# Kernel optimization log

Hardware: AMD Instinct MI355X
Metric: run time of the kernel (lower is better)

## Reference

```python
import jax, jax.numpy as jnp
import numpy as np

B, K, HH, WW = 512, 256, 16, 16   # batch, channels (K//2 of init K=512), latent H, W
KH = 128                          # GRU hidden size
F = 16                            # future_window_lin


def gru_forward(seq, h0, W_ih, W_hh, b_ih, b_hh):
    # seq: (B,T,K) batch_first, h0: (B,KH). PyTorch GRU gate order: r, z, n.
    gx = jnp.einsum('btk,gk->btg', seq, W_ih) + b_ih  # (B,T,3*KH)

    def step(h, gx_t):
        gh = h @ W_hh.T + b_hh
        xr, xz, xn = jnp.split(gx_t, 3, axis=-1)
        hr, hz, hn = jnp.split(gh, 3, axis=-1)
        r = jax.nn.sigmoid(xr + hr)
        z = jax.nn.sigmoid(xz + hz)
        n = jnp.tanh(xn + r * hn)
        h_new = (1.0 - z) * n + z * h
        return h_new, h_new

    hT, outs = jax.lax.scan(step, h0, jnp.swapaxes(gx, 0, 1))  # outs: (T,B,KH)
    return jnp.swapaxes(outs, 0, 1), hT


def setup_inputs() -> dict:
    key = jax.random.key(0)
    ks = jax.random.split(key, 9)
    s = 0.05
    return {
        'z_q_x_st': jax.random.normal(ks[0], (B, K, HH, WW), jnp.float32),
        'z_e_x': jax.random.normal(ks[1], (B, K, HH, WW), jnp.float32),
        'z_q_x': jax.random.normal(ks[2], (B, K, HH, WW), jnp.float32),
        'hidden': jnp.zeros((1, B, KH), jnp.float32),
        'W_ih': jax.random.normal(ks[3], (3 * KH, K), jnp.float32) * s,
        'W_hh': jax.random.normal(ks[4], (3 * KH, KH), jnp.float32) * s,
        'b_ih': jnp.zeros((3 * KH,), jnp.float32),
        'b_hh': jnp.zeros((3 * KH,), jnp.float32),
        'Wk_w': jax.random.normal(ks[5], (F, K, KH), jnp.float32) * s,
        'Wk_b': jnp.zeros((F, K), jnp.float32),
        'p_sample': 100,
    }


def reference(z_q_x_st, z_e_x, z_q_x, hidden, W_ih, W_hh, b_ih, b_hh, Wk_w, Wk_b, p_sample):
    batch, k, h, w = z_e_x.shape
    f = Wk_w.shape[0]
    # (B,K,H,W) -> (B,H*W,K); row = idx//W, col = idx%W is just the row-major flat index
    z_flat = jnp.transpose(z_q_x_st, (0, 2, 3, 1)).reshape(batch, h * w, k)
    # encoded samples at flat positions p_sample+1 .. p_sample+F  -> (F,B,K)
    encoded = jnp.swapaxes(z_flat[:, p_sample + 1: p_sample + 1 + f, :], 0, 1)
    # GRU over the causal prefix; c_t = output at step p_sample (the last one)
    seq = z_flat[:, : p_sample + 1, :]
    out, _ = gru_forward(seq, hidden[0], W_ih, W_hh, b_ih, b_hh)
    c_t = out[:, -1, :]  # (B,KH)
    # per-step linear heads, batched: (F,B,K)
    pred = jnp.einsum('fkh,bh->fbk', Wk_w, c_t) + Wk_b[:, None, :]
    # totals[i] = encoded[i] @ pred[i].T  -> (F,B,B)
    totals = jnp.einsum('fbk,fck->fbc', encoded, pred)
    lsm = jax.nn.log_softmax(totals, axis=2)
    diag_sum = jnp.sum(jnp.diagonal(lsm, axis1=1, axis2=2))
    nce = -diag_sum / (batch * f)
    # 'correct' only reflects the last loop iteration in the torch code
    last = totals[-1]
    sm = jax.nn.softmax(last, axis=1)       # softmax over dim=1, then argmax over dim=0
    preds_idx = jnp.argmax(sm, axis=0)
    correct = jnp.sum(preds_idx == jnp.arange(batch))
    accuracy = correct.astype(jnp.float32) / batch
    return accuracy, nce, z_e_x, z_q_x
```

## Files before the change

kernel.cpp:

```cpp
#include <hip/hip_runtime.h>
#include <math.h>

#define NB_B   512
#define NK     256
#define NKH    128
#define NG3    384
#define NT     101
#define NF     16
#define NPASS  (512ull*256*256)

#define OFF_GX   0ull
#define N_GX     (512ull*101*384)
#define OFF_CT   (OFF_GX + N_GX)
#define OFF_ENC  (OFF_CT + 512ull*128)
#define OFF_PRED (OFF_ENC + 16ull*512*256)
#define OFF_TOT  (OFF_PRED + 16ull*512*256)
#define OFF_LSE  (OFF_TOT + 16ull*512*512)
#define OFF_DML  (OFF_LSE + 8192ull)
#define OFF_WT   (OFF_DML + 8192ull)
#define OFF_WKT  (OFF_WT + 384ull*256)
#define OFF_CNT  (OFF_WKT + 16ull*128*256)

__global__ __launch_bounds__(256) void k_transpose(
    const float* __restrict__ W_ih, const float* __restrict__ Wk_w,
    float* __restrict__ Wt, float* __restrict__ Wkt, int* __restrict__ cnt) {
  int idx = blockIdx.x * 256 + threadIdx.x;
  if (idx == 0) *cnt = 0;
  if (idx < 384 * 256) {
    int g = idx % 384, k = idx / 384;
    Wt[idx] = W_ih[g * 256 + k];
  }
  if (idx < 16 * 128 * 256) {
    int k = idx & 255, h = (idx >> 8) & 127, f = idx >> 15;
    Wkt[idx] = Wk_w[(f * 256 + k) * 128 + h];
  }
}

__global__ __launch_bounds__(768) void k_gx(
    const float* __restrict__ zq, const float* __restrict__ Wt,
    const float* __restrict__ b_ih, float* __restrict__ gx) {
  __shared__ float Xs[32][104];
  __shared__ float Ws[32 * 384];
  int b = blockIdx.x;
  int tid = threadIdx.x;
  int q = tid % 96;
  int tt = tid / 96;
  int g0 = q * 4;
  int t0 = tt * 13;
  int lane = tid & 63, wid = tid >> 6;
  float acc[4][13];
#pragma unroll
  for (int i = 0; i < 4; i++)
#pragma unroll
    for (int j = 0; j < 13; j++) acc[i][j] = 0.f;
  const float* zb = zq + (size_t)b * 65536;
  for (int kc = 0; kc < 8; kc++) {
    __syncthreads();
    for (int k = wid; k < 32; k += 12) {
      int kk = kc * 32 + k;
      Xs[k][lane] = zb[kk * 256 + lane];
      int t1 = 64 + lane;
      if (t1 < 104) Xs[k][t1] = (t1 < 101) ? zb[kk * 256 + t1] : 0.f;
    }
    {
      const float4* wsrc = (const float4*)(Wt + (size_t)kc * 32 * 384);
      float4* wdst = (float4*)Ws;
      for (int i = tid; i < 3072; i += 768) wdst[i] = wsrc[i];
    }
    __syncthreads();
    for (int k = 0; k < 32; k++) {
      float4 w = *(const float4*)&Ws[k * 384 + g0];
      const float* xr = &Xs[k][t0];
#pragma unroll
      for (int j = 0; j < 13; j++) {
        float x = xr[j];
        acc[0][j] += w.x * x;
        acc[1][j] += w.y * x;
        acc[2][j] += w.z * x;
        acc[3][j] += w.w * x;
      }
    }
  }
  float4 bias = *(const float4*)&b_ih[g0];
#pragma unroll
  for (int j = 0; j < 13; j++) {
    int t = t0 + j;
    if (t < 101) {
      float4 v = make_float4(acc[0][j] + bias.x, acc[1][j] + bias.y,
                             acc[2][j] + bias.z, acc[3][j] + bias.w);
      *(float4*)&gx[(size_t)t * (512 * 384) + b * 384 + g0] = v;
    }
  }
}

__global__ __launch_bounds__(768) void k_scan(
    const float* __restrict__ gx, const float* __restrict__ W_hh,
    const float* __restrict__ b_hh, const float* __restrict__ hidden,
    float* __restrict__ ct,
    const float* __restrict__ src0, const float* __restrict__ src1,
    float2* __restrict__ d0, float2* __restrict__ d1) {
  int tid = threadIdx.x;
  if (blockIdx.x >= 256) {
    const float2* S0 = (const float2*)src0;
    const float2* S1 = (const float2*)src1;
    const size_t half = NPASS / 4;
    const size_t stride = 256ull * 768;
    for (size_t i = (size_t)(blockIdx.x - 256) * 768 + tid; i < half; i += stride) {
      float2 a = S0[i];
      float2 b2 = S0[i + half];
      float2 c = S1[i];
      float2 d = S1[i + half];
      d0[i] = a;
      d0[i + half] = b2;
      d1[i] = c;
      d1[i + half] = d;
    }
    return;
  }
  __shared__ float hs[2][128];
  __shared__ float ghp[2][2][384];
  int b0 = blockIdx.x * 2;
  int g = tid % 384, kh = tid / 384;
  float4 w[16];
  const float4* wp = (const float4*)(W_hh + g * 128 + kh * 64);
#pragma unroll
  for (int i = 0; i < 16; i++) w[i] = wp[i];
  if (tid < 256) {
    int r = tid >> 7, k = tid & 127;
    hs[r][k] = hidden[(b0 + r) * 128 + k];
  }
  __syncthreads();
  for (int t = 0; t < 101; t++) {
    const float4* h0 = (const float4*)&hs[0][kh * 64];
    const float4* h1 = (const float4*)&hs[1][kh * 64];
    float a0 = 0.f, a1 = 0.f;
#pragma unroll
    for (int i = 0; i < 16; i++) {
      float4 wv = w[i], x0 = h0[i], x1 = h1[i];
      a0 += wv.x * x0.x + wv.y * x0.y + wv.z * x0.z + wv.w * x0.w;
      a1 += wv.x * x1.x + wv.y * x1.y + wv.z * x1.z + wv.w * x1.w;
    }
    ghp[0][kh][g] = a0;
    ghp[1][kh][g] = a1;
    __syncthreads();
    if (tid < 256) {
      int r = tid >> 7, k = tid & 127;
      const float* gxb = gx + (size_t)t * (512 * 384) + (b0 + r) * 384;
      float xr = gxb[k], xz = gxb[128 + k], xn = gxb[256 + k];
      float hr = ghp[r][0][k] + ghp[r][1][k] + b_hh[k];
      float hz = ghp[r][0][128 + k] + ghp[r][1][128 + k] + b_hh[128 + k];
      float hn = ghp[r][0][256 + k] + ghp[r][1][256 + k] + b_hh[256 + k];
      float rr = 1.f / (1.f + __expf(-(xr + hr)));
      float zz = 1.f / (1.f + __expf(-(xz + hz)));
      float nn = tanhf(xn + rr * hn);
      hs[r][k] = (1.f - zz) * nn + zz * hs[r][k];
    }
    __syncthreads();
  }
  if (tid < 256) {
    int r = tid >> 7, k = tid & 127;
    ct[(b0 + r) * 128 + k] = hs[r][k];
  }
}

__global__ __launch_bounds__(256) void k_enc(const float* __restrict__ zq,
                                             float* __restrict__ enc) {
  __shared__ float tile[256][17];
  int b = blockIdx.x, tid = threadIdx.x;
  const float* zb = zq + (size_t)b * 65536;
  for (int pass = 0; pass < 16; pass++) {
    int idx = pass * 256 + tid;
    int k = idx >> 4, f = idx & 15;
    tile[k][f] = zb[k * 256 + 101 + f];
  }
  __syncthreads();
  for (int f = 0; f < 16; f++)
    enc[(size_t)f * 131072 + b * 256 + tid] = tile[tid][f];
}

__global__ __launch_bounds__(256) void k_pred(
    const float* __restrict__ Wkt, const float* __restrict__ Wk_b,
    const float* __restrict__ ct, float* __restrict__ pred) {
  __shared__ float cts[32][128];
  int f = blockIdx.x, c0 = blockIdx.y * 32;
  int tid = threadIdx.x;
  for (int pass = 0; pass < 16; pass++) {
    int idx = pass * 256 + tid;
    int cc = idx >> 7, h = idx & 127;
    cts[cc][h] = ct[(c0 + cc) * 128 + h];
  }
  __syncthreads();
  float acc[32];
#pragma unroll
  for (int i = 0; i < 32; i++) acc[i] = 0.f;
  const float* wb = Wkt + (size_t)f * 32768 + tid;
  for (int h = 0; h < 128; h += 4) {
    float w0 = wb[(h + 0) * 256], w1 = wb[(h + 1) * 256];
    float w2 = wb[(h + 2) * 256], w3 = wb[(h + 3) * 256];
#pragma unroll
    for (int cc = 0; cc < 32; cc++) {
      float4 cv = *(const float4*)&cts[cc][h];
      acc[cc] += w0 * cv.x + w1 * cv.y + w2 * cv.z + w3 * cv.w;
    }
  }
  float bias = Wk_b[f * 256 + tid];
#pragma unroll
  for (int cc = 0; cc < 32; cc++)
    pred[((size_t)f * 512 + c0 + cc) * 256 + tid] = acc[cc] + bias;
}

__global__ __launch_bounds__(256) void k_totals(
    const float* __restrict__ enc, const float* __restrict__ pred,
    float* __restrict__ tot) {
  __shared__ float As[32][68];
  __shared__ float Bs[32][68];
  int f = blockIdx.z, b0 = blockIdx.y * 64, c0 = blockIdx.x * 64;
  int tid = threadIdx.x;
  int tx = tid & 15, ty = tid >> 4;
  float acc[4][4];
#pragma unroll
  for (int i = 0; i < 4; i++)
#pragma unroll
    for (int j = 0; j < 4; j++) acc[i][j] = 0.f;
  const float* Ab = enc + (size_t)f * 131072;
  const float* Bb = pred + (size_t)f * 131072;
  int lr = tid >> 3;
  int lc = (tid & 7) * 4;
  for (int kc = 0; kc < 8; kc++) {
    int k0 = kc * 32;
    __syncthreads();
    float4 av0 = *(const float4*)&Ab[(b0 + lr) * 256 + k0 + lc];
    float4 av1 = *(const float4*)&Ab[(b0 + 32 + lr) * 256 + k0 + lc];
    float4 bv0 = *(const float4*)&Bb[(c0 + lr) * 256 + k0 + lc];
    float4 bv1 = *(const float4*)&Bb[(c0 + 32 + lr) * 256 + k0 + lc];
    As[lc + 0][lr] = av0.x; As[lc + 1][lr] = av0.y;
    As[lc + 2][lr] = av0.z; As[lc + 3][lr] = av0.w;
    As[lc + 0][lr + 32] = av1.x; As[lc + 1][lr + 32] = av1.y;
    As[lc + 2][lr + 32] = av1.z; As[lc + 3][lr + 32] = av1.w;
    Bs[lc + 0][lr] = bv0.x; Bs[lc + 1][lr] = bv0.y;
    Bs[lc + 2][lr] = bv0.z; Bs[lc + 3][lr] = bv0.w;
    Bs[lc + 0][lr + 32] = bv1.x; Bs[lc + 1][lr + 32] = bv1.y;
    Bs[lc + 2][lr + 32] = bv1.z; Bs[lc + 3][lr + 32] = bv1.w;
    __syncthreads();
#pragma unroll
    for (int kk = 0; kk < 32; kk++) {
      float4 a = *(const float4*)&As[kk][ty * 4];
      float4 bq = *(const float4*)&Bs[kk][tx * 4];
      acc[0][0] += a.x * bq.x; acc[0][1] += a.x * bq.y;
      acc[0][2] += a.x * bq.z; acc[0][3] += a.x * bq.w;
      acc[1][0] += a.y * bq.x; acc[1][1] += a.y * bq.y;
      acc[1][2] += a.y * bq.z; acc[1][3] += a.y * bq.w;
      acc[2][0] += a.z * bq.x; acc[2][1] += a.z * bq.y;
      acc[2][2] += a.z * bq.z; acc[2][3] += a.z * bq.w;
      acc[3][0] += a.w * bq.x; acc[3][1] += a.w * bq.y;
      acc[3][2] += a.w * bq.z; acc[3][3] += a.w * bq.w;
    }
  }
#pragma unroll
  for (int i = 0; i < 4; i++) {
    float4 v = make_float4(acc[i][0], acc[i][1], acc[i][2], acc[i][3]);
    *(float4*)&tot[(size_t)f * 262144 + (b0 + ty * 4 + i) * 512 + c0 + tx * 4] = v;
  }
}

__global__ __launch_bounds__(64) void k_lse(const float* __restrict__ tot,
                                            float* __restrict__ lse,
                                            float* __restrict__ dml) {
  int row = blockIdx.x;
  int b = row & 511;
  int lane = threadIdx.x;
  const float* tr = tot + (size_t)row * 512;
  float v[8];
  float mx = -1e30f;
#pragma unroll
  for (int i = 0; i < 8; i++) { v[i] = tr[i * 64 + lane]; mx = fmaxf(mx, v[i]); }
#pragma unroll
  for (int s = 32; s > 0; s >>= 1) mx = fmaxf(mx, __shfl_xor(mx, s));
  float sum = 0.f;
#pragma unroll
  for (int i = 0; i < 8; i++) sum += __expf(v[i] - mx);
#pragma unroll
  for (int s = 32; s > 0; s >>= 1) sum += __shfl_xor(sum, s);
  if (lane == 0) {
    float l = __logf(sum) + mx;
    lse[row] = l;
    dml[row] = tr[b] - l;
  }
}

__global__ __launch_bounds__(64) void k_acc(const float* __restrict__ tot,
                                            const float* __restrict__ lse,
                                            int* __restrict__ cnt) {
  int c = blockIdx.x;
  int lane = threadIdx.x;
  const float* t15 = tot + (size_t)15 * 262144;
  const float* l15 = lse + 15 * 512;
  float best = -1e30f;
  int bi = 1 << 30;
  for (int b = lane; b < 512; b += 64) {
    float v = t15[(size_t)b * 512 + c] - l15[b];
    if (v > best) { best = v; bi = b; }
  }
  for (int s = 32; s > 0; s >>= 1) {
    float ov = __shfl_xor(best, s);
    int oi = __shfl_xor(bi, s);
    if (ov > best || (ov == best && oi < bi)) { best = ov; bi = oi; }
  }
  if (lane == 0 && bi == c) atomicAdd(cnt, 1);
}

__global__ __launch_bounds__(256) void k_fin(const float* __restrict__ dml,
                                             const int* __restrict__ cnt,
                                             float* __restrict__ out) {
  __shared__ float red[256];
  int tid = threadIdx.x;
  float s = 0.f;
  for (int i = tid; i < 8192; i += 256) s += dml[i];
  red[tid] = s;
  __syncthreads();
  for (int st = 128; st > 0; st >>= 1) {
    if (tid < st) red[tid] += red[tid + st];
    __syncthreads();
  }
  if (tid == 0) {
    out[1] = -red[0] / 8192.f;
    out[0] = (float)(*cnt) / 512.f;
  }
}

extern "C" void kernel_launch(void* const* d_in, const int* in_sizes, int n_in,
                              void* d_out, int out_size, void* d_ws, size_t ws_size,
                              hipStream_t stream) {
  const float* zq   = (const float*)d_in[0];
  const float* ze   = (const float*)d_in[1];
  const float* zqx  = (const float*)d_in[2];
  const float* hid  = (const float*)d_in[3];
  const float* W_ih = (const float*)d_in[4];
  const float* W_hh = (const float*)d_in[5];
  const float* b_ih = (const float*)d_in[6];
  const float* b_hh = (const float*)d_in[7];
  const float* Wk_w = (const float*)d_in[8];
  const float* Wk_b = (const float*)d_in[9];
  float* out = (float*)d_out;
  float* ws  = (float*)d_ws;

  k_transpose<<<2048, 256, 0, stream>>>(W_ih, Wk_w, ws + OFF_WT, ws + OFF_WKT,
                                        (int*)(ws + OFF_CNT));
  k_gx<<<512, 768, 0, stream>>>(zq, ws + OFF_WT, b_ih, ws + OFF_GX);
  k_scan<<<512, 768, 0, stream>>>(ws + OFF_GX, W_hh, b_hh, hid, ws + OFF_CT,
                                  ze, zqx,
                                  (float2*)(out + 2), (float2*)(out + 2 + NPASS));
  k_enc<<<512, 256, 0, stream>>>(zq, ws + OFF_ENC);
  k_pred<<<dim3(16, 16), 256, 0, stream>>>(ws + OFF_WKT, Wk_b, ws + OFF_CT, ws + OFF_PRED);
  k_totals<<<dim3(8, 8, 16), 256, 0, stream>>>(ws + OFF_ENC, ws + OFF_PRED, ws + OFF_TOT);
  k_lse<<<8192, 64, 0, stream>>>(ws + OFF_TOT, ws + OFF_LSE, ws + OFF_DML);
  k_acc<<<512, 64, 0, stream>>>(ws + OFF_TOT, ws + OFF_LSE, (int*)(ws + OFF_CNT));
  k_fin<<<1, 256, 0, stream>>>(ws + OFF_DML, (const int*)(ws + OFF_CNT), out);
}
```

Measured before the change: 913.5 us.

## Interleave passthrough copy into GRU scan blocks and use readlane broadcasts

```diff
diff --git a/kernel.cpp b/kernel.cpp
--- a/kernel.cpp
+++ b/kernel.cpp
@@ -38,7 +38,8 @@
 
 __global__ __launch_bounds__(768) void k_gx(
     const float* __restrict__ zq, const float* __restrict__ Wt,
-    const float* __restrict__ b_ih, float* __restrict__ gx) {
+    const float* __restrict__ b_ih, const float* __restrict__ b_hh,
+    float* __restrict__ gx) {
   __shared__ float Xs[32][104];
   __shared__ float Ws[32 * 384];
   int b = blockIdx.x;
@@ -82,6 +83,10 @@
     }
   }
   float4 bias = *(const float4*)&b_ih[g0];
+  if (g0 + 3 < 256) {
+    bias.x += b_hh[g0 + 0]; bias.y += b_hh[g0 + 1];
+    bias.z += b_hh[g0 + 2]; bias.w += b_hh[g0 + 3];
+  }
 #pragma unroll
   for (int j = 0; j < 13; j++) {
     int t = t0 + j;
@@ -93,73 +98,102 @@
   }
 }
 
-__global__ __launch_bounds__(768) void k_scan(
+__global__ __launch_bounds__(1024, 4) void k_scan(
     const float* __restrict__ gx, const float* __restrict__ W_hh,
     const float* __restrict__ b_hh, const float* __restrict__ hidden,
     float* __restrict__ ct,
     const float* __restrict__ src0, const float* __restrict__ src1,
     float2* __restrict__ d0, float2* __restrict__ d1) {
-  int tid = threadIdx.x;
-  if (blockIdx.x >= 256) {
-    const float2* S0 = (const float2*)src0;
-    const float2* S1 = (const float2*)src1;
-    const size_t half = NPASS / 4;
-    const size_t stride = 256ull * 768;
-    for (size_t i = (size_t)(blockIdx.x - 256) * 768 + tid; i < half; i += stride) {
-      float2 a = S0[i];
-      float2 b2 = S0[i + half];
-      float2 c = S1[i];
-      float2 d = S1[i + half];
-      d0[i] = a;
-      d0[i + half] = b2;
-      d1[i] = c;
-      d1[i + half] = d;
-    }
-    return;
-  }
   __shared__ float hs[2][128];
   __shared__ float ghp[2][2][384];
+  int tid = threadIdx.x;
   int b0 = blockIdx.x * 2;
-  int g = tid % 384, kh = tid / 384;
-  float4 w[16];
-  const float4* wp = (const float4*)(W_hh + g * 128 + kh * 64);
-#pragma unroll
-  for (int i = 0; i < 16; i++) w[i] = wp[i];
-  if (tid < 256) {
-    int r = tid >> 7, k = tid & 127;
-    hs[r][k] = hidden[(b0 + r) * 128 + k];
-  }
-  __syncthreads();
-  for (int t = 0; t < 101; t++) {
-    const float4* h0 = (const float4*)&hs[0][kh * 64];
-    const float4* h1 = (const float4*)&hs[1][kh * 64];
-    float a0 = 0.f, a1 = 0.f;
+  bool copy_role = (tid >= 768);
+
+  int kh = tid / 384;
+  int g = tid % 384;
+  int lane = tid & 63;
+  float w[64];
+  float cxr = 0.f, cxz = 0.f, cxn = 0.f, nxr = 0.f, nxz = 0.f, nxn = 0.f;
+  float bhn = 0.f;
+  const float2* S0 = (const float2*)src0;
+  const float2* S1 = (const float2*)src1;
+  int c = tid - 768;
+  size_t sbase = (size_t)blockIdx.x * 65536;
+  int p = 0;
+
+  if (!copy_role) {
+    const float* wp = W_hh + g * 128 + kh * 64;
 #pragma unroll
     for (int i = 0; i < 16; i++) {
-      float4 wv = w[i], x0 = h0[i], x1 = h1[i];
-      a0 += wv.x * x0.x + wv.y * x0.y + wv.z * x0.z + wv.w * x0.w;
-      a1 += wv.x * x1.x + wv.y * x1.y + wv.z * x1.z + wv.w * x1.w;
-    }
-    ghp[0][kh][g] = a0;
-    ghp[1][kh][g] = a1;
-    __syncthreads();
+      float4 v = *(const float4*)(wp + 4 * i);
+      w[4 * i + 0] = v.x; w[4 * i + 1] = v.y;
+      w[4 * i + 2] = v.z; w[4 * i + 3] = v.w;
+    }
     if (tid < 256) {
       int r = tid >> 7, k = tid & 127;
-      const float* gxb = gx + (size_t)t * (512 * 384) + (b0 + r) * 384;
-      float xr = gxb[k], xz = gxb[128 + k], xn = gxb[256 + k];
-      float hr = ghp[r][0][k] + ghp[r][1][k] + b_hh[k];
-      float hz = ghp[r][0][128 + k] + ghp[r][1][128 + k] + b_hh[128 + k];
-      float hn = ghp[r][0][256 + k] + ghp[r][1][256 + k] + b_hh[256 + k];
-      float rr = 1.f / (1.f + __expf(-(xr + hr)));
-      float zz = 1.f / (1.f + __expf(-(xz + hz)));
-      float nn = tanhf(xn + rr * hn);
+      hs[r][k] = hidden[(b0 + r) * 128 + k];
+      bhn = b_hh[256 + k];
+      const float* gxb = gx + (b0 + r) * 384;
+      cxr = gxb[k]; cxz = gxb[128 + k]; cxn = gxb[256 + k];
+    }
+  }
+  __syncthreads();
+
+  for (int t = 0; t < 101; t++) {
+    if (!copy_role) {
+      float hr0 = hs[0][kh * 64 + lane];
+      float hr1 = hs[1][kh * 64 + lane];
+      float a0 = 0.f, a1 = 0.f;
+#pragma unroll
+      for (int j = 0; j < 64; j++) {
+        float h0 = __int_as_float(__builtin_amdgcn_readlane(__float_as_int(hr0), j));
+        float h1 = __int_as_float(__builtin_amdgcn_readlane(__float_as_int(hr1), j));
+        a0 = fmaf(w[j], h0, a0);
+        a1 = fmaf(w[j], h1, a1);
+      }
+      ghp[0][kh][g] = a0;
+      ghp[1][kh][g] = a1;
+      if (tid < 256 && t < 100) {
+        int r = tid >> 7, k = tid & 127;
+        const float* gxb = gx + (size_t)(t + 1) * (512 * 384) + (b0 + r) * 384;
+        nxr = gxb[k]; nxz = gxb[128 + k]; nxn = gxb[256 + k];
+      }
+    } else {
+#pragma unroll
+      for (int uu = 0; uu < 5; uu++) {
+        int u = p + uu;
+        size_t idx = sbase + (size_t)(u >> 1) * 256 + c;
+        if (u & 1) d1[idx] = S1[idx];
+        else       d0[idx] = S0[idx];
+      }
+      p += 5;
+    }
+    __syncthreads();
+    if (!copy_role && tid < 256) {
+      int r = tid >> 7, k = tid & 127;
+      float hrr = ghp[r][0][k] + ghp[r][1][k];
+      float hzz = ghp[r][0][128 + k] + ghp[r][1][128 + k];
+      float hnn = ghp[r][0][256 + k] + ghp[r][1][256 + k] + bhn;
+      float rr = 1.f / (1.f + __expf(-(cxr + hrr)));
+      float zz = 1.f / (1.f + __expf(-(cxz + hzz)));
+      float nn = tanhf(cxn + rr * hnn);
       hs[r][k] = (1.f - zz) * nn + zz * hs[r][k];
-    }
-    __syncthreads();
-  }
-  if (tid < 256) {
+      cxr = nxr; cxz = nxz; cxn = nxn;
+    }
+    __syncthreads();
+  }
+
+  if (!copy_role && tid < 256) {
     int r = tid >> 7, k = tid & 127;
     ct[(b0 + r) * 128 + k] = hs[r][k];
+  }
+  if (copy_role) {
+    for (; p < 512; p++) {
+      size_t idx = sbase + (size_t)(p >> 1) * 256 + c;
+      if (p & 1) d1[idx] = S1[idx];
+      else       d0[idx] = S0[idx];
+    }
   }
 }
 
@@ -346,10 +380,10 @@
 
   k_transpose<<<2048, 256, 0, stream>>>(W_ih, Wk_w, ws + OFF_WT, ws + OFF_WKT,
                                         (int*)(ws + OFF_CNT));
-  k_gx<<<512, 768, 0, stream>>>(zq, ws + OFF_WT, b_ih, ws + OFF_GX);
-  k_scan<<<512, 768, 0, stream>>>(ws + OFF_GX, W_hh, b_hh, hid, ws + OFF_CT,
-                                  ze, zqx,
-                                  (float2*)(out + 2), (float2*)(out + 2 + NPASS));
+  k_gx<<<512, 768, 0, stream>>>(zq, ws + OFF_WT, b_ih, b_hh, ws + OFF_GX);
+  k_scan<<<256, 1024, 0, stream>>>(ws + OFF_GX, W_hh, b_hh, hid, ws + OFF_CT,
+                                   ze, zqx,
+                                   (float2*)(out + 2), (float2*)(out + 2 + NPASS));
   k_enc<<<512, 256, 0, stream>>>(zq, ws + OFF_ENC);
   k_pred<<<dim3(16, 16), 256, 0, stream>>>(ws + OFF_WKT, Wk_b, ws + OFF_CT, ws + OFF_PRED);
   k_totals<<<dim3(8, 8, 16), 256, 0, stream>>>(ws + OFF_ENC, ws + OFF_PRED, ws + OFF_TOT);
```

Result: no change. 912.5 us (-0.1%).
